# Optimization experiments

Hardware: AMD Instinct MI355X
Metric: run time of the kernel (lower is better)

The kernel has to match this reference:

```python
import jax, jax.numpy as jnp
import numpy as np

N_NODES = 100000
N_EDGES = 1600000
NEG_SLOPE = 0.2


def _gat_conv(x, src, dst, W, att_src, att_dst, bias, heads, out_ch):
    """PyG-style GATConv (eval mode, self-loops already in src/dst)."""
    n = x.shape[0]
    h = (x @ W).reshape(n, heads, out_ch)            # [N,H,C]
    a_src = jnp.sum(h * att_src, axis=-1)            # [N,H]
    a_dst = jnp.sum(h * att_dst, axis=-1)            # [N,H]
    e = jax.nn.leaky_relu(a_src[src] + a_dst[dst], NEG_SLOPE)  # [E,H]
    # segment softmax over destination nodes
    m = jax.ops.segment_max(e, dst, num_segments=n)  # [N,H]
    ex = jnp.exp(e - m[dst])                         # [E,H]
    denom = jax.ops.segment_sum(ex, dst, num_segments=n)  # [N,H]
    alpha = ex / (denom[dst] + 1e-16)                # [E,H]
    # weighted scatter-aggregate of source features
    out = jax.ops.segment_sum(alpha[:, :, None] * h[src], dst, num_segments=n)  # [N,H,C]
    return out.reshape(n, heads * out_ch) + bias


def setup_inputs() -> dict:
    key = jax.random.key(0)
    ks = jax.random.split(key, 10)
    nfeat, nhid, nclass, heads = 128, 16, 40, 8
    return {
        "x": jax.random.normal(ks[0], (N_NODES, nfeat), jnp.float32),
        "edge_index": jax.random.randint(ks[1], (2, N_EDGES), 0, N_NODES, jnp.int64),
        "W1": jax.random.normal(ks[2], (nfeat, heads * nhid), jnp.float32) * 0.1,
        "att_src1": jax.random.normal(ks[3], (1, heads, nhid), jnp.float32) * 0.1,
        "att_dst1": jax.random.normal(ks[4], (1, heads, nhid), jnp.float32) * 0.1,
        "b1": jax.random.normal(ks[5], (heads * nhid,), jnp.float32) * 0.1,
        "W2": jax.random.normal(ks[6], (heads * nhid, nclass), jnp.float32) * 0.1,
        "att_src2": jax.random.normal(ks[7], (1, 1, nclass), jnp.float32) * 0.1,
        "att_dst2": jax.random.normal(ks[8], (1, 1, nclass), jnp.float32) * 0.1,
        "b2": jax.random.normal(ks[9], (nclass,), jnp.float32) * 0.1,
    }


def reference(x, edge_index, W1, att_src1, att_dst1, b1, W2, att_src2, att_dst2, b2):
    n = x.shape[0]
    # add self loops (PyG GATConv default)
    loops = jnp.arange(n, dtype=edge_index.dtype)
    src = jnp.concatenate([edge_index[0], loops])
    dst = jnp.concatenate([edge_index[1], loops])
    # dropout p=0.6 is a no-op in eval mode
    h = _gat_conv(x, src, dst, W1, att_src1, att_dst1, b1, heads=8, out_ch=16)
    h = jax.nn.elu(h)
    out = _gat_conv(h, src, dst, W2, att_src2, att_dst2, b2, heads=1, out_ch=40)
    return jax.nn.log_softmax(out, axis=1)
```

## Files before the change

### kernel.cpp

```cpp
#include <hip/hip_runtime.h>
#include <math.h>


#define NPB   32
#define G     8
#define RCAP  192
#define BSTRIDE (G*RCAP)

__device__ __forceinline__ float wave_max(float v){
  #pragma unroll
  for (int m = 1; m < 64; m <<= 1) v = fmaxf(v, __shfl_xor(v, m));
  return v;
}
__device__ __forceinline__ float wave_sum(float v){
  #pragma unroll
  for (int m = 1; m < 64; m <<= 1) v += __shfl_xor(v, m);
  return v;
}
__device__ __forceinline__ void lds_fence(){
  asm volatile("s_waitcnt lgkmcnt(0)" ::: "memory");
  __builtin_amdgcn_sched_barrier(0);
}

__device__ __forceinline__ unsigned short f2bf(float f){
  unsigned int u = __float_as_uint(f);
  u += 0x7FFFu + ((u >> 16) & 1u);
  return (unsigned short)(u >> 16);
}
__device__ __forceinline__ float bf2f(unsigned short b){
  return __uint_as_float(((unsigned int)b) << 16);
}
__device__ __forceinline__ float2 bfpair(unsigned int u){
  float2 r;
  r.x = __uint_as_float(u << 16);
  r.y = __uint_as_float(u & 0xFFFF0000u);
  return r;
}


__global__ void zero_bcnt_kernel(int* __restrict__ p, int nr){
  int i = blockIdx.x * 256 + threadIdx.x;
  if (i < nr) p[i] = 0;
}

__global__ void binA_kernel(const int* __restrict__ src, const int* __restrict__ dst,
                            int* __restrict__ bcnt, unsigned int* __restrict__ bdata,
                            int E, int tot){
  int i = blockIdx.x * 256 + threadIdx.x;
  if (i >= tot) return;
  int s, d;
  if (i < E){ s = src[i]; d = dst[i]; } else { s = i - E; d = s; }
  int b = d >> 5;
  int r = b * G + (blockIdx.x & (G - 1));
  int pos = atomicAdd(&bcnt[r], 1);
  if (pos < RCAP)
    bdata[(size_t)r * RCAP + pos] = (unsigned int)s | ((unsigned int)(d & 31) << 17);
}

__global__ __launch_bounds__(256)
void binB_kernel(const int* __restrict__ bcnt, const unsigned int* __restrict__ bdata,
                 int* __restrict__ offs, int* __restrict__ cntg,
                 int* __restrict__ col, int n){
  __shared__ int hist[NPB];
  __shared__ int sc[NPB];
  __shared__ int curp[NPB];
  int tid = threadIdx.x;
  int b = blockIdx.x;
  int base_node = b * NPB;

  if (tid < NPB) hist[tid] = 0;
  __syncthreads();
  #pragma unroll
  for (int g = 0; g < G; g++){
    int rc = bcnt[b * G + g]; if (rc > RCAP) rc = RCAP;
    size_t rb = (size_t)(b * G + g) * RCAP;
    for (int j = tid; j < rc; j += 256)
      atomicAdd(&hist[bdata[rb + j] >> 17], 1);
  }
  __syncthreads();
  if (tid < NPB) sc[tid] = hist[tid];
  __syncthreads();
  #pragma unroll
  for (int d1 = 1; d1 < NPB; d1 <<= 1){
    int v = 0;
    if (tid < NPB && tid >= d1) v = sc[tid - d1];
    __syncthreads();
    if (tid < NPB) sc[tid] += v;
    __syncthreads();
  }
  if (tid < NPB){
    int ex = tid ? sc[tid - 1] : 0;
    int node = base_node + tid;
    if (node < n){
      offs[node] = b * BSTRIDE + ex;
      cntg[node] = hist[tid];
    }
    curp[tid] = ex;
  }
  __syncthreads();
  #pragma unroll
  for (int g = 0; g < G; g++){
    int rc = bcnt[b * G + g]; if (rc > RCAP) rc = RCAP;
    size_t rb = (size_t)(b * G + g) * RCAP;
    for (int j = tid; j < rc; j += 256){
      unsigned int u = bdata[rb + j];
      int r = atomicAdd(&curp[u >> 17], 1);
      col[b * BSTRIDE + r] = (int)(u & 0x1FFFFu);
    }
  }
}

__global__ __launch_bounds__(256)
void gemm1_kernel(const float* __restrict__ X, const float* __restrict__ W,
                  unsigned short* __restrict__ Hb, int n){
  __shared__ float xs[16][132];
  __shared__ float ws[16][128];
  int tid = threadIdx.x;
  int rg = tid >> 4, cg = tid & 15;
  int r0 = rg * 8, c0 = cg * 4;
  int row0 = blockIdx.x * 128;
  float acc[8][8];
  #pragma unroll
  for (int i = 0; i < 8; i++)
    #pragma unroll
    for (int j = 0; j < 8; j++) acc[i][j] = 0.f;

  for (int k0 = 0; k0 < 128; k0 += 16){
    #pragma unroll
    for (int l = 0; l < 2; l++){
      int f4 = tid + l * 256;
      int kk = f4 >> 5, cq = f4 & 31;
      float4 w = *(const float4*)(W + (size_t)(k0 + kk) * 128 + cq * 4);
      *(float4*)&ws[kk][cq * 4] = w;
    }
    #pragma unroll
    for (int l = 0; l < 2; l++){
      int f4 = tid + l * 256;
      int row = f4 >> 2, kq = f4 & 3;
      float4 v = make_float4(0.f, 0.f, 0.f, 0.f);
      if (row0 + row < n)
        v = *(const float4*)(X + (size_t)(row0 + row) * 128 + k0 + kq * 4);
      xs[kq*4+0][row] = v.x; xs[kq*4+1][row] = v.y;
      xs[kq*4+2][row] = v.z; xs[kq*4+3][row] = v.w;
    }
    __syncthreads();
    #pragma unroll
    for (int k = 0; k < 16; k++){
      float4 xa = *(const float4*)&xs[k][r0];
      float4 xb = *(const float4*)&xs[k][r0 + 4];
      float4 wa = *(const float4*)&ws[k][c0];
      float4 wb = *(const float4*)&ws[k][c0 + 64];
      float xr[8] = {xa.x,xa.y,xa.z,xa.w,xb.x,xb.y,xb.z,xb.w};
      float wr[8] = {wa.x,wa.y,wa.z,wa.w,wb.x,wb.y,wb.z,wb.w};
      #pragma unroll
      for (int i = 0; i < 8; i++)
        #pragma unroll
        for (int j = 0; j < 8; j++)
          acc[i][j] = fmaf(xr[i], wr[j], acc[i][j]);
    }
    __syncthreads();
  }
  #pragma unroll
  for (int i = 0; i < 8; i++){
    int r = row0 + r0 + i;
    if (r < n){
      ushort4 a4, b4;
      a4.x = f2bf(acc[i][0]); a4.y = f2bf(acc[i][1]);
      a4.z = f2bf(acc[i][2]); a4.w = f2bf(acc[i][3]);
      b4.x = f2bf(acc[i][4]); b4.y = f2bf(acc[i][5]);
      b4.z = f2bf(acc[i][6]); b4.w = f2bf(acc[i][7]);
      *(ushort4*)(Hb + (size_t)r * 128 + c0)      = a4;
      *(ushort4*)(Hb + (size_t)r * 128 + c0 + 64) = b4;
    }
  }
}

__global__ __launch_bounds__(256)
void att1_kernel(const unsigned short* __restrict__ Hb, const float* __restrict__ As,
                 const float* __restrict__ Ad, float* __restrict__ asrc,
                 float* __restrict__ adst, int n){
  __shared__ float sa[128], sd[128];
  int tid = threadIdx.x;
  if (tid < 128){ sa[tid] = As[tid]; sd[tid] = Ad[tid]; }
  __syncthreads();
  int t = blockIdx.x * 256 + tid;
  if (t >= n * 8) return;
  int node = t >> 3, h = t & 7;
  const uint4* hp = (const uint4*)(Hb + (size_t)node * 128 + h * 16);
  uint4 u0 = hp[0], u1 = hp[1];
  unsigned int w[8] = {u0.x,u0.y,u0.z,u0.w,u1.x,u1.y,u1.z,u1.w};
  float s = 0.f, d = 0.f;
  #pragma unroll
  for (int q = 0; q < 8; q++){
    float2 p = bfpair(w[q]);
    s = fmaf(p.x, sa[h*16 + 2*q],     s);
    s = fmaf(p.y, sa[h*16 + 2*q + 1], s);
    d = fmaf(p.x, sd[h*16 + 2*q],     d);
    d = fmaf(p.y, sd[h*16 + 2*q + 1], d);
  }
  asrc[t] = s; adst[t] = d;
}

#define CAP1 64
__global__ __launch_bounds__(256)
void agg1_kernel(const unsigned short* __restrict__ Hb, const int* __restrict__ offs,
                 const int* __restrict__ cnt, const int* __restrict__ col,
                 const float* __restrict__ asrc, const float* __restrict__ adst,
                 const float* __restrict__ bias, float* __restrict__ G1, int n){
  __shared__ int   scol[4][CAP1];
  __shared__ float sex[4][CAP1][8];
  int lane = threadIdx.x & 63;
  int wid  = threadIdx.x >> 6;
  int node = blockIdx.x * 4 + wid;
  if (node >= n) return;
  int beg = offs[node], deg = cnt[node];

  int hA = lane & 7, iA = lane >> 3;
  int hB = lane >> 3;
  float adA = adst[node * 8 + hA];

  float2 acc = make_float2(0.f, 0.f);
  float m_run = -INFINITY;
  float denomA = 0.f;

  for (int c0 = 0; c0 < deg; c0 += CAP1){
    int cdeg = min(CAP1, deg - c0);
    float ev[8];
    float cm = -INFINITY;
    #pragma unroll
    for (int k = 0; k < 8; k++){
      int i = iA + k * 8;
      ev[k] = -INFINITY;
      if (i < cdeg){
        int s = col[beg + c0 + i];
        if (hA == 0) scol[wid][i] = s;
        float e = asrc[s * 8 + hA] + adA;
        e = e > 0.f ? e : 0.2f * e;
        ev[k] = e;
        cm = fmaxf(cm, e);
      }
    }
    cm = fmaxf(cm, __shfl_xor(cm, 8));
    cm = fmaxf(cm, __shfl_xor(cm, 16));
    cm = fmaxf(cm, __shfl_xor(cm, 32));
    float m_new = fmaxf(m_run, cm);
    float scaleA = __expf(m_run - m_new);
    denomA *= scaleA;
    #pragma unroll
    for (int k = 0; k < 8; k++){
      int i = iA + k * 8;
      if (i < cdeg){
        float ex = __expf(ev[k] - m_new);
        denomA += ex;
        sex[wid][i][hA] = ex;
      }
    }
    m_run = m_new;
    float scaleB = __shfl(scaleA, hB);
    acc.x *= scaleB; acc.y *= scaleB;
    lds_fence();
    const unsigned int* Hu = (const unsigned int*)Hb;
    int i = 0;
    for (; i + 7 < cdeg; i += 8){
      int ss[8]; float xx[8]; unsigned int uu[8];
      #pragma unroll
      for (int k = 0; k < 8; k++){
        ss[k] = scol[wid][i + k];
        xx[k] = sex[wid][i + k][hB];
      }
      #pragma unroll
      for (int k = 0; k < 8; k++)
        uu[k] = Hu[(size_t)ss[k] * 64 + lane];
      #pragma unroll
      for (int k = 0; k < 8; k++){
        float2 f = bfpair(uu[k]);
        acc.x = fmaf(xx[k], f.x, acc.x);
        acc.y = fmaf(xx[k], f.y, acc.y);
      }
    }
    for (; i < cdeg; i++){
      int s = scol[wid][i];
      float x = sex[wid][i][hB];
      float2 f = bfpair(Hu[(size_t)s * 64 + lane]);
      acc.x = fmaf(x, f.x, acc.x);
      acc.y = fmaf(x, f.y, acc.y);
    }
  }
  denomA += __shfl_xor(denomA, 8);
  denomA += __shfl_xor(denomA, 16);
  denomA += __shfl_xor(denomA, 32);
  float denomB = __shfl(denomA, hB) + 1e-16f;
  float2 bv = ((const float2*)bias)[lane];
  float ox = acc.x / denomB + bv.x;
  float oy = acc.y / denomB + bv.y;
  ox = ox > 0.f ? ox : expm1f(ox);
  oy = oy > 0.f ? oy : expm1f(oy);
  ((float2*)G1)[(size_t)node * 64 + lane] = make_float2(ox, oy);
}

__global__ __launch_bounds__(256)
void gemm2_kernel(const float* __restrict__ X, const float* __restrict__ W,
                  unsigned short* __restrict__ Hb, int n){
  __shared__ float xs[16][132];
  __shared__ float ws[16][48];
  int tid = threadIdx.x;
  int rg = tid >> 3, cg = tid & 7;
  int r0 = rg * 4, c0 = cg * 6;
  int row0 = blockIdx.x * 128;
  float acc[4][6];
  #pragma unroll
  for (int i = 0; i < 4; i++)
    #pragma unroll
    for (int j = 0; j < 6; j++) acc[i][j] = 0.f;

  for (int k0 = 0; k0 < 128; k0 += 16){
    #pragma unroll
    for (int l = 0; l < 3; l++){
      int idx = tid + l * 256;
      int kk = idx / 48, c = idx % 48;
      ws[kk][c] = (c < 40) ? W[(size_t)(k0 + kk) * 40 + c] : 0.f;
    }
    #pragma unroll
    for (int l = 0; l < 2; l++){
      int f4 = tid + l * 256;
      int row = f4 >> 2, kq = f4 & 3;
      float4 v = make_float4(0.f, 0.f, 0.f, 0.f);
      if (row0 + row < n)
        v = *(const float4*)(X + (size_t)(row0 + row) * 128 + k0 + kq * 4);
      xs[kq*4+0][row] = v.x; xs[kq*4+1][row] = v.y;
      xs[kq*4+2][row] = v.z; xs[kq*4+3][row] = v.w;
    }
    __syncthreads();
    #pragma unroll
    for (int k = 0; k < 16; k++){
      float4 xa = *(const float4*)&xs[k][r0];
      float xr[4] = {xa.x, xa.y, xa.z, xa.w};
      float wr[6];
      #pragma unroll
      for (int j = 0; j < 6; j++) wr[j] = ws[k][c0 + j];
      #pragma unroll
      for (int i = 0; i < 4; i++)
        #pragma unroll
        for (int j = 0; j < 6; j++)
          acc[i][j] = fmaf(xr[i], wr[j], acc[i][j]);
    }
    __syncthreads();
  }
  #pragma unroll
  for (int i = 0; i < 4; i++){
    int r = row0 + r0 + i;
    if (r < n){
      #pragma unroll
      for (int j = 0; j < 6; j++){
        int c = c0 + j;
        if (c < 40) Hb[(size_t)r * 40 + c] = f2bf(acc[i][j]);
      }
    }
  }
}

__global__ __launch_bounds__(256)
void att2_kernel(const unsigned short* __restrict__ Hb, const float* __restrict__ As,
                 const float* __restrict__ Ad, float* __restrict__ asrc,
                 float* __restrict__ adst, int n){
  int lane = threadIdx.x & 63;
  int node = blockIdx.x * 4 + (threadIdx.x >> 6);
  if (node >= n) return;
  float v = 0.f, a = 0.f, d = 0.f;
  if (lane < 40){
    v = bf2f(Hb[(size_t)node * 40 + lane]);
    a = As[lane];
    d = Ad[lane];
  }
  float s1 = wave_sum(v * a);
  float s2 = wave_sum(v * d);
  if (lane == 0){ asrc[node] = s1; adst[node] = s2; }
}

#define CAP2 128
__global__ __launch_bounds__(256)
void agg2_kernel(const unsigned short* __restrict__ Hb, const int* __restrict__ offs,
                 const int* __restrict__ cnt, const int* __restrict__ col,
                 const float* __restrict__ asrc, const float* __restrict__ adst,
                 const float* __restrict__ bias, float* __restrict__ out, int n){
  __shared__ int   scol[4][CAP2];
  __shared__ float sex[4][CAP2];
  int lane = threadIdx.x & 63;
  int wid  = threadIdx.x >> 6;
  int node = blockIdx.x * 4 + wid;
  if (node >= n) return;
  int beg = offs[node], deg = cnt[node];
  float ad = adst[node];

  float acc = 0.f;
  float m_run = -INFINITY;
  float denom = 0.f;

  for (int c0 = 0; c0 < deg; c0 += CAP2){
    int cdeg = min(CAP2, deg - c0);
    float ev[2];
    float cm = -INFINITY;
    #pragma unroll
    for (int k = 0; k < 2; k++){
      int i = lane + k * 64;
      ev[k] = -INFINITY;
      if (i < cdeg){
        int s = col[beg + c0 + i];
        scol[wid][i] = s;
        float e = asrc[s] + ad;
        e = e > 0.f ? e : 0.2f * e;
        ev[k] = e;
        cm = fmaxf(cm, e);
      }
    }
    cm = wave_max(cm);
    float m_new = fmaxf(m_run, cm);
    float scale = __expf(m_run - m_new);
    float part = 0.f;
    #pragma unroll
    for (int k = 0; k < 2; k++){
      int i = lane + k * 64;
      if (i < cdeg){
        float ex = __expf(ev[k] - m_new);
        part += ex;
        sex[wid][i] = ex;
      }
    }
    denom = denom * scale + wave_sum(part);
    acc *= scale;
    m_run = m_new;
    lds_fence();
    int i = 0;
    for (; i + 7 < cdeg; i += 8){
      int ss[8]; float xx[8]; float ff[8];
      #pragma unroll
      for (int k = 0; k < 8; k++){
        ss[k] = scol[wid][i + k];
        xx[k] = sex[wid][i + k];
      }
      #pragma unroll
      for (int k = 0; k < 8; k++)
        ff[k] = (lane < 40) ? bf2f(Hb[(size_t)ss[k] * 40 + lane]) : 0.f;
      #pragma unroll
      for (int k = 0; k < 8; k++)
        acc = fmaf(xx[k], ff[k], acc);
    }
    for (; i < cdeg; i++){
      int s = scol[wid][i];
      float x = sex[wid][i];
      float f = (lane < 40) ? bf2f(Hb[(size_t)s * 40 + lane]) : 0.f;
      acc = fmaf(x, f, acc);
    }
  }
  float val = 0.f;
  if (lane < 40) val = acc / (denom + 1e-16f) + bias[lane];

  float mx = wave_max(lane < 40 ? val : -INFINITY);
  float ssum = wave_sum(lane < 40 ? __expf(val - mx) : 0.f);
  float ls = logf(ssum);
  if (lane < 40) out[(size_t)node * 40 + lane] = val - mx - ls;
}

extern "C" void kernel_launch(void* const* d_in, const int* in_sizes, int n_in,
                              void* d_out, int out_size, void* d_ws, size_t ws_size,
                              hipStream_t stream){
  const float* x   = (const float*)d_in[0];
  const int*   ei  = (const int*)d_in[1];
  const float* W1  = (const float*)d_in[2];
  const float* as1 = (const float*)d_in[3];
  const float* ad1 = (const float*)d_in[4];
  const float* b1  = (const float*)d_in[5];
  const float* W2  = (const float*)d_in[6];
  const float* as2 = (const float*)d_in[7];
  const float* ad2 = (const float*)d_in[8];
  const float* b2  = (const float*)d_in[9];
  float* out = (float*)d_out;

  int n = in_sizes[0] / 128;
  int E = in_sizes[1] / 2;
  const int* src = ei;
  const int* dst = ei + E;
  int tot = E + n;
  int nb = (n + NPB - 1) / NPB;
  int nr = nb * G;

  char* w = (char*)d_ws;
  size_t off = 0;
  auto alloc = [&](size_t bytes){
    size_t r = off; off += (bytes + 255) & ~(size_t)255; return r;
  };
  int* bcnt = (int*)(w + alloc((size_t)nr * 4));
  unsigned int* bdata = (unsigned int*)(w + alloc((size_t)nr * RCAP * 4));
  int* offs = (int*)(w + alloc((size_t)n * 4));
  int* cnt  = (int*)(w + alloc((size_t)n * 4));
  int* col  = (int*)(w + alloc((size_t)nb * BSTRIDE * 4));
  unsigned short* h1b = (unsigned short*)(w + alloc((size_t)n * 128 * 2));
  float* g1   = (float*)(w + alloc((size_t)n * 128 * 4));
  float* s1   = (float*)(w + alloc((size_t)n * 8 * 4));
  float* t1   = (float*)(w + alloc((size_t)n * 8 * 4));
  unsigned short* h2b = h1b;
  float* s2 = s1;
  float* t2 = t1;
  (void)ws_size; (void)n_in; (void)out_size;

  zero_bcnt_kernel<<<(nr + 255) / 256, 256, 0, stream>>>(bcnt, nr);
  binA_kernel<<<(tot + 255) / 256, 256, 0, stream>>>(src, dst, bcnt, bdata, E, tot);
  binB_kernel<<<nb, 256, 0, stream>>>(bcnt, bdata, offs, cnt, col, n);

  gemm1_kernel<<<(n + 127) / 128, 256, 0, stream>>>(x, W1, h1b, n);
  att1_kernel<<<(n * 8 + 255) / 256, 256, 0, stream>>>(h1b, as1, ad1, s1, t1, n);
  agg1_kernel<<<(n + 3) / 4, 256, 0, stream>>>(h1b, offs, cnt, col, s1, t1, b1, g1, n);

  gemm2_kernel<<<(n + 127) / 128, 256, 0, stream>>>(g1, W2, h2b, n);
  att2_kernel<<<(n + 3) / 4, 256, 0, stream>>>(h2b, as2, ad2, s2, t2, n);
  agg2_kernel<<<(n + 3) / 4, 256, 0, stream>>>(h2b, offs, cnt, col, s2, t2, b2, out, n);
}
```

Measured before the change: 546.3 us.

## Replace LDS staging in aggregation kernels with register lane broadcasts

Both aggregation kernels stop staging neighbor indices and softmax weights in shared memory. They broadcast them from registers with readlane and shfl instead. This removes the LDS writes and reads and the waitcnt fence. Edges are processed in padded groups of 8, so out-of-range slots gather row 0 with a zero weight. Indexing also moves to 32-bit unsigned arithmetic. The cost is some wasted gathers on partial groups and more cross-lane instructions per edge.

```diff
diff --git a/kernel.cpp b/kernel.cpp
--- a/kernel.cpp
+++ b/kernel.cpp
@@ -17,9 +17,11 @@
   for (int m = 1; m < 64; m <<= 1) v += __shfl_xor(v, m);
   return v;
 }
-__device__ __forceinline__ void lds_fence(){
-  asm volatile("s_waitcnt lgkmcnt(0)" ::: "memory");
-  __builtin_amdgcn_sched_barrier(0);
+__device__ __forceinline__ int lane_bcast_i(int v, int l){
+  return __builtin_amdgcn_readlane(v, l);
+}
+__device__ __forceinline__ float lane_bcast_f(float v, int l){
+  return __uint_as_float((unsigned)__builtin_amdgcn_readlane(__float_as_int(v), l));
 }
 
 __device__ __forceinline__ unsigned short f2bf(float f){
@@ -201,14 +203,11 @@
   asrc[t] = s; adst[t] = d;
 }
 
-#define CAP1 64
 __global__ __launch_bounds__(256)
 void agg1_kernel(const unsigned short* __restrict__ Hb, const int* __restrict__ offs,
                  const int* __restrict__ cnt, const int* __restrict__ col,
                  const float* __restrict__ asrc, const float* __restrict__ adst,
                  const float* __restrict__ bias, float* __restrict__ G1, int n){
-  __shared__ int   scol[4][CAP1];
-  __shared__ float sex[4][CAP1][8];
   int lane = threadIdx.x & 63;
   int wid  = threadIdx.x >> 6;
   int node = blockIdx.x * 4 + wid;
@@ -217,26 +216,27 @@
 
   int hA = lane & 7, iA = lane >> 3;
   int hB = lane >> 3;
-  float adA = adst[node * 8 + hA];
+  float adA = adst[(unsigned)node * 8u + hA];
+  const unsigned int* Hu = (const unsigned int*)Hb;
 
   float2 acc = make_float2(0.f, 0.f);
   float m_run = -INFINITY;
   float denomA = 0.f;
 
-  for (int c0 = 0; c0 < deg; c0 += CAP1){
-    int cdeg = min(CAP1, deg - c0);
-    float ev[8];
+  for (int c0 = 0; c0 < deg; c0 += 64){
+    int cdeg = min(64, deg - c0);
+    int sv[8]; float xv[8];
     float cm = -INFINITY;
     #pragma unroll
     for (int k = 0; k < 8; k++){
       int i = iA + k * 8;
-      ev[k] = -INFINITY;
+      sv[k] = 0; xv[k] = -INFINITY;
       if (i < cdeg){
         int s = col[beg + c0 + i];
-        if (hA == 0) scol[wid][i] = s;
-        float e = asrc[s * 8 + hA] + adA;
+        sv[k] = s;
+        float e = asrc[(unsigned)s * 8u + hA] + adA;
         e = e > 0.f ? e : 0.2f * e;
-        ev[k] = e;
+        xv[k] = e;
         cm = fmaxf(cm, e);
       }
     }
@@ -250,40 +250,25 @@
     for (int k = 0; k < 8; k++){
       int i = iA + k * 8;
       if (i < cdeg){
-        float ex = __expf(ev[k] - m_new);
+        float ex = __expf(xv[k] - m_new);
+        xv[k] = ex;
         denomA += ex;
-        sex[wid][i][hA] = ex;
-      }
+      } else xv[k] = 0.f;
     }
     m_run = m_new;
     float scaleB = __shfl(scaleA, hB);
     acc.x *= scaleB; acc.y *= scaleB;
-    lds_fence();
-    const unsigned int* Hu = (const unsigned int*)Hb;
-    int i = 0;
-    for (; i + 7 < cdeg; i += 8){
-      int ss[8]; float xx[8]; unsigned int uu[8];
-      #pragma unroll
-      for (int k = 0; k < 8; k++){
-        ss[k] = scol[wid][i + k];
-        xx[k] = sex[wid][i + k][hB];
+    #pragma unroll
+    for (int k = 0; k < 8; k++){
+      if (k * 8 >= cdeg) break;
+      #pragma unroll
+      for (int j = 0; j < 8; j++){
+        int sk = lane_bcast_i(sv[k], j * 8);
+        float exk = __shfl(xv[k], j * 8 + hB);
+        float2 f = bfpair(Hu[(unsigned)sk * 64u + lane]);
+        acc.x = fmaf(exk, f.x, acc.x);
+        acc.y = fmaf(exk, f.y, acc.y);
       }
-      #pragma unroll
-      for (int k = 0; k < 8; k++)
-        uu[k] = Hu[(size_t)ss[k] * 64 + lane];
-      #pragma unroll
-      for (int k = 0; k < 8; k++){
-        float2 f = bfpair(uu[k]);
-        acc.x = fmaf(xx[k], f.x, acc.x);
-        acc.y = fmaf(xx[k], f.y, acc.y);
-      }
-    }
-    for (; i < cdeg; i++){
-      int s = scol[wid][i];
-      float x = sex[wid][i][hB];
-      float2 f = bfpair(Hu[(size_t)s * 64 + lane]);
-      acc.x = fmaf(x, f.x, acc.x);
-      acc.y = fmaf(x, f.y, acc.y);
     }
   }
   denomA += __shfl_xor(denomA, 8);
@@ -377,79 +362,49 @@
   if (lane == 0){ asrc[node] = s1; adst[node] = s2; }
 }
 
-#define CAP2 128
 __global__ __launch_bounds__(256)
 void agg2_kernel(const unsigned short* __restrict__ Hb, const int* __restrict__ offs,
                  const int* __restrict__ cnt, const int* __restrict__ col,
                  const float* __restrict__ asrc, const float* __restrict__ adst,
                  const float* __restrict__ bias, float* __restrict__ out, int n){
-  __shared__ int   scol[4][CAP2];
-  __shared__ float sex[4][CAP2];
   int lane = threadIdx.x & 63;
   int wid  = threadIdx.x >> 6;
   int node = blockIdx.x * 4 + wid;
   if (node >= n) return;
   int beg = offs[node], deg = cnt[node];
   float ad = adst[node];
+  unsigned choff = (lane < 40) ? (unsigned)lane : 0u;
 
   float acc = 0.f;
   float m_run = -INFINITY;
   float denom = 0.f;
 
-  for (int c0 = 0; c0 < deg; c0 += CAP2){
-    int cdeg = min(CAP2, deg - c0);
-    float ev[2];
-    float cm = -INFINITY;
-    #pragma unroll
-    for (int k = 0; k < 2; k++){
-      int i = lane + k * 64;
-      ev[k] = -INFINITY;
-      if (i < cdeg){
-        int s = col[beg + c0 + i];
-        scol[wid][i] = s;
-        float e = asrc[s] + ad;
-        e = e > 0.f ? e : 0.2f * e;
-        ev[k] = e;
-        cm = fmaxf(cm, e);
-      }
-    }
-    cm = wave_max(cm);
+  for (int c0 = 0; c0 < deg; c0 += 64){
+    int cdeg = min(64, deg - c0);
+    int s = 0; float ev = -INFINITY;
+    if (lane < cdeg){
+      s = col[beg + c0 + lane];
+      float e = asrc[s] + ad;
+      ev = e > 0.f ? e : 0.2f * e;
+    }
+    float cm = wave_max(ev);
     float m_new = fmaxf(m_run, cm);
     float scale = __expf(m_run - m_new);
-    float part = 0.f;
-    #pragma unroll
-    for (int k = 0; k < 2; k++){
-      int i = lane + k * 64;
-      if (i < cdeg){
-        float ex = __expf(ev[k] - m_new);
-        part += ex;
-        sex[wid][i] = ex;
-      }
-    }
-    denom = denom * scale + wave_sum(part);
+    float ex = (lane < cdeg) ? __expf(ev - m_new) : 0.f;
+    denom = denom * scale + wave_sum(ex);
     acc *= scale;
     m_run = m_new;
-    lds_fence();
-    int i = 0;
-    for (; i + 7 < cdeg; i += 8){
-      int ss[8]; float xx[8]; float ff[8];
-      #pragma unroll
-      for (int k = 0; k < 8; k++){
-        ss[k] = scol[wid][i + k];
-        xx[k] = sex[wid][i + k];
+    #pragma unroll
+    for (int kb = 0; kb < 8; kb++){
+      if (kb * 8 >= cdeg) break;
+      #pragma unroll
+      for (int j = 0; j < 8; j++){
+        int k = kb * 8 + j;
+        int sk = lane_bcast_i(s, k);
+        float exk = lane_bcast_f(ex, k);
+        float f = bf2f(Hb[(unsigned)sk * 40u + choff]);
+        acc = fmaf(exk, f, acc);
       }
-      #pragma unroll
-      for (int k = 0; k < 8; k++)
-        ff[k] = (lane < 40) ? bf2f(Hb[(size_t)ss[k] * 40 + lane]) : 0.f;
-      #pragma unroll
-      for (int k = 0; k < 8; k++)
-        acc = fmaf(xx[k], ff[k], acc);
-    }
-    for (; i < cdeg; i++){
-      int s = scol[wid][i];
-      float x = sex[wid][i];
-      float f = (lane < 40) ? bf2f(Hb[(size_t)s * 40 + lane]) : 0.f;
-      acc = fmaf(x, f, acc);
     }
   }
   float val = 0.f;
```

Result: faster. 502.7 us (-8.0%).
